# Optimization experiments

Hardware: AMD Instinct MI355X
Metric: run time of the kernel (lower is better)

## Reference

```python
import jax, jax.numpy as jnp
import numpy as np

N, FEAT, D, H, C, FF, PH, E = 50000, 64, 128, 4, 32, 512, 256, 600000
LN_EPS = 1e-5
NEG_SLOPE = 0.2


def layer_norm(x, g, b):
    m = x.mean(-1, keepdims=True)
    v = ((x - m) ** 2).mean(-1, keepdims=True)
    return (x - m) * jax.lax.rsqrt(v + LN_EPS) * g + b


def gat_conv(x, edge_index, W, a_src, a_dst, bias):
    # PyG GATConv, concat=True, add_self_loops=True, negative_slope=0.2, eval mode.
    n = x.shape[0]
    h = (x @ W).reshape(n, H, C)                       # [N,H,C]
    al_s = jnp.einsum('nhc,hc->nh', h, a_src)          # [N,H]
    al_d = jnp.einsum('nhc,hc->nh', h, a_dst)
    loops = jnp.arange(n)
    src = jnp.concatenate([edge_index[0], loops])      # [E+N]
    dst = jnp.concatenate([edge_index[1], loops])
    alpha = jax.nn.leaky_relu(al_s[src] + al_d[dst], NEG_SLOPE)  # [E+N,H]
    amax = jax.lax.stop_gradient(jax.ops.segment_max(alpha, dst, num_segments=n))
    ex = jnp.exp(alpha - amax[dst])
    denom = jax.ops.segment_sum(ex, dst, num_segments=n)
    w = ex / denom[dst]                                # segment softmax over incoming edges
    msg = h[src] * w[:, :, None]                       # [E+N,H,C]
    out = jax.ops.segment_sum(msg, dst, num_segments=n).reshape(n, H * C)
    return out + bias


def encoder_layer(x, ei, W, a_s, a_d, b, W1, b1, W2, b2, g1, bt1, g2, bt2):
    h = gat_conv(x, ei, W, a_s, a_d, b)
    x = layer_norm(x + h, g1, bt1)
    f = jax.nn.relu(x @ W1 + b1) @ W2 + b2
    return layer_norm(x + f, g2, bt2)


def setup_inputs() -> dict:
    key = jax.random.key(0)
    ks = iter(jax.random.split(key, 64))
    rn = lambda shp, s=0.08: jax.random.normal(next(ks), shp, dtype=jnp.float32) * s
    d = {}
    d['x'] = jax.random.normal(next(ks), (N, FEAT), dtype=jnp.float32)
    d['edge_index'] = jax.random.randint(next(ks), (2, E), 0, N)
    d['virtual_edge_index'] = jax.random.randint(next(ks), (2, E), 0, N)
    d['Wp'] = rn((FEAT, D)); d['bp'] = jnp.zeros((D,))
    d['lnp_g'] = jnp.ones((D,)); d['lnp_b'] = jnp.zeros((D,))
    for p in ('v', 'r'):
        d[p + 'W'] = rn((2, D, D)); d[p + '_as'] = rn((2, H, C), 0.1); d[p + '_ad'] = rn((2, H, C), 0.1)
        d[p + '_b'] = jnp.zeros((2, D))
        d[p + 'W1'] = rn((2, D, FF)); d[p + 'b1'] = jnp.zeros((2, FF))
        d[p + 'W2'] = rn((2, FF, D)); d[p + 'b2'] = jnp.zeros((2, D))
        d[p + 'ln1g'] = jnp.ones((2, D)); d[p + 'ln1b'] = jnp.zeros((2, D))
        d[p + 'ln2g'] = jnp.ones((2, D)); d[p + 'ln2b'] = jnp.zeros((2, D))
    d['We1'] = rn((2 * D, PH)); d['be1'] = jnp.zeros((PH,))
    d['We2'] = rn((PH, 1)); d['be2'] = jnp.zeros((1,))
    return d


def reference(x, edge_index, virtual_edge_index, Wp, bp, lnp_g, lnp_b,
              vW, v_as, v_ad, v_b, vW1, vb1, vW2, vb2, vln1g, vln1b, vln2g, vln2b,
              rW, r_as, r_ad, r_b, rW1, rb1, rW2, rb2, rln1g, rln1b, rln2g, rln2b,
              We1, be1, We2, be2):
    # preprocessing
    h = layer_norm(jax.nn.relu(x @ Wp + bp), lnp_g, lnp_b)
    # virtual-link encoders
    for i in range(vW.shape[0]):
        h = encoder_layer(h, virtual_edge_index, vW[i], v_as[i], v_ad[i], v_b[i],
                          vW1[i], vb1[i], vW2[i], vb2[i], vln1g[i], vln1b[i], vln2g[i], vln2b[i])
    # real-link encoders
    for i in range(rW.shape[0]):
        h = encoder_layer(h, edge_index, rW[i], r_as[i], r_ad[i], r_b[i],
                          rW1[i], rb1[i], rW2[i], rb2[i], rln1g[i], rln1b[i], rln2g[i], rln2b[i])
    # edge predictor
    ef = jnp.concatenate([h[edge_index[0]], h[edge_index[1]]], axis=-1)  # [E,2D]
    flow = (jax.nn.relu(ef @ We1 + be1) @ We2 + be2)[:, 0]
    return jax.nn.relu(flow)
```

## Files before the change

### kernel.cpp

```cpp
#include <hip/hip_runtime.h>
#include <hip/hip_bf16.h>
#include <math.h>

#define NODES 50000
#define NFEAT 64
#define DIM 128
#define HEADS 4
#define CHC 32
#define FFDIM 512
#define PHDIM 256
#define NEDGE 600000
#define LN_EPS 1e-5f
#define SLOPE 0.2f

typedef __attribute__((ext_vector_type(8))) short bf16x8;
typedef __attribute__((ext_vector_type(4))) float f32x4;
typedef __attribute__((ext_vector_type(4))) unsigned short us4;

__device__ __forceinline__ unsigned short f2bf(float f) {
    __hip_bfloat16 h = __float2bfloat16(f);
    return reinterpret_cast<unsigned short&>(h);
}
__device__ __forceinline__ float bf2f(unsigned short u) {
    return __uint_as_float(((unsigned int)u) << 16);
}

__device__ __forceinline__ void ln_stats128(float val, float* red, float& mean, float& rstd) {
    float s1 = val, s2 = val * val;
#pragma unroll
    for (int off = 32; off > 0; off >>= 1) {
        s1 += __shfl_xor(s1, off, 64);
        s2 += __shfl_xor(s2, off, 64);
    }
    int wv = threadIdx.x >> 6;
    if ((threadIdx.x & 63) == 0) { red[wv * 2] = s1; red[wv * 2 + 1] = s2; }
    __syncthreads();
    float t1 = red[0] + red[2];
    float t2 = red[1] + red[3];
    mean = t1 * (1.f / 128.f);
    float var = t2 * (1.f / 128.f) - mean * mean;
    rstd = rsqrtf(var + LN_EPS);
}

__global__ void k_count2(const int* __restrict__ dstV, const int* __restrict__ dstR,
                         int* __restrict__ cntV, int* __restrict__ cntR) {
    int e = blockIdx.x * 256 + threadIdx.x;
    if (e < NEDGE) atomicAdd(&cntV[dstV[e]], 1);
    else if (e < 2 * NEDGE) atomicAdd(&cntR[dstR[e - NEDGE]], 1);
}

__global__ void k_scan2(const int* __restrict__ degV, int* __restrict__ rpV,
                        const int* __restrict__ degR, int* __restrict__ rpR) {
    __shared__ int sh[1024];
    const int* deg = blockIdx.x ? degR : degV;
    int* rp = blockIdx.x ? rpR : rpV;
    int t = threadIdx.x;
    const int per = (NODES + 1023) / 1024;
    int beg = t * per;
    int end = beg + per; if (end > NODES) end = NODES; if (beg > NODES) beg = NODES;
    int s = 0;
    for (int i = beg; i < end; i++) s += deg[i];
    sh[t] = s;
    __syncthreads();
    for (int off = 1; off < 1024; off <<= 1) {
        int v = (t >= off) ? sh[t - off] : 0;
        __syncthreads();
        sh[t] += v;
        __syncthreads();
    }
    int run = sh[t] - s;
    for (int i = beg; i < end; i++) { rp[i] = run; run += deg[i]; }
    if (t == 1023) rp[NODES] = sh[1023];
}

__global__ void k_fill2(const int* __restrict__ eiV, const int* __restrict__ eiR,
                        const int* __restrict__ rpV, const int* __restrict__ rpR,
                        int* __restrict__ cntV, int* __restrict__ cntR,
                        int* __restrict__ ciV, int* __restrict__ ciR) {
    int e = blockIdx.x * 256 + threadIdx.x;
    if (e < NEDGE) {
        int s = eiV[e], d = eiV[NEDGE + e];
        int pos = atomicAdd(&cntV[d], 1);
        ciV[rpV[d] + pos] = s;
    } else if (e < 2 * NEDGE) {
        int e2 = e - NEDGE;
        int s = eiR[e2], d = eiR[NEDGE + e2];
        int pos = atomicAdd(&cntR[d], 1);
        ciR[rpR[d] + pos] = s;
    }
}

template <int KI, int NR>
__global__ void k_wcvt2b(const float* __restrict__ inV, const float* __restrict__ inR,
                         unsigned short* __restrict__ oh, unsigned short* __restrict__ ol,
                         size_t ostride) {
    int l = blockIdx.y;
    const float* in = (l < 2 ? inV : inR) + (size_t)(l & 1) * KI * NR;
    unsigned short* ohp = oh + (size_t)l * ostride;
    unsigned short* olp = ol + (size_t)l * ostride;
    int tid = blockIdx.x * 256 + threadIdx.x;
    int n = tid / KI, k = tid % KI;
    float w = in[k * NR + n];
    unsigned short h = f2bf(w);
    ohp[tid] = h;
    olp[tid] = f2bf(w - bf2f(h));
}

__global__ void k_wcvt_pq(const float* __restrict__ We1, unsigned short* __restrict__ oh,
                          unsigned short* __restrict__ ol) {
    int tid = blockIdx.x * 256 + threadIdx.x;
    int n = tid >> 7, k = tid & 127;
    float w = (n < PHDIM) ? We1[k * PHDIM + n] : We1[(DIM + k) * PHDIM + (n - PHDIM)];
    unsigned short h = f2bf(w);
    oh[tid] = h;
    ol[tid] = f2bf(w - bf2f(h));
}

__global__ void k_preprocess(const float* __restrict__ x0, const float* __restrict__ Wp,
                             const float* __restrict__ bp, const float* __restrict__ g,
                             const float* __restrict__ b, float* __restrict__ xout) {
    __shared__ float xr[NFEAT];
    __shared__ float red[4];
    int n = blockIdx.x;
    int j = threadIdx.x;
    if (j < NFEAT) xr[j] = x0[n * NFEAT + j];
    __syncthreads();
    float acc = bp[j];
#pragma unroll
    for (int k = 0; k < NFEAT; k++) acc += xr[k] * Wp[k * DIM + j];
    acc = fmaxf(acc, 0.f);
    float mean, rstd;
    ln_stats128(acc, red, mean, rstd);
    xout[n * DIM + j] = (acc - mean) * rstd * g[j] + b[j];
}

#define XS_STRIDE 136
#define HID_STRIDE 520
#define FB_STRIDE 132
#define MFMA_BF16 __builtin_amdgcn_mfma_f32_16x16x32_bf16

__global__ void k_xw_mfma(const float* __restrict__ x,
                          const unsigned short* __restrict__ Wh,
                          const unsigned short* __restrict__ Wl,
                          const float* __restrict__ a_s, const float* __restrict__ a_d,
                          unsigned short* __restrict__ hg, float* __restrict__ als,
                          float* __restrict__ ald) {
    __shared__ __align__(16) unsigned short xsh[32 * XS_STRIDE];
    __shared__ __align__(16) unsigned short xsl[32 * XS_STRIDE];
    int t = threadIdx.x;
    int n0 = blockIdx.x * 32;

#pragma unroll
    for (int jj = 0; jj < 4; jj++) {
        int v = t + jj * 256;
        int m = v >> 5, c4 = (v & 31) * 4;
        int node = n0 + m;
        float4 f;
        if (node < NODES) f = *(const float4*)(x + (size_t)node * DIM + c4);
        else { f.x = f.y = f.z = f.w = 0.f; }
        us4 uh = {f2bf(f.x), f2bf(f.y), f2bf(f.z), f2bf(f.w)};
        us4 ul = {f2bf(f.x - bf2f(uh.x)), f2bf(f.y - bf2f(uh.y)),
                  f2bf(f.z - bf2f(uh.z)), f2bf(f.w - bf2f(uh.w))};
        *(us4*)(xsh + m * XS_STRIDE + c4) = uh;
        *(us4*)(xsl + m * XS_STRIDE + c4) = ul;
    }
    __syncthreads();

    int wv = t >> 6, l = t & 63, lr = l & 15, lk = l >> 4;

    f32x4 acc[2][2];
#pragma unroll
    for (int mf = 0; mf < 2; mf++)
#pragma unroll
        for (int nf = 0; nf < 2; nf++) acc[mf][nf] = (f32x4){0.f, 0.f, 0.f, 0.f};
#pragma unroll
    for (int kk = 0; kk < 4; kk++) {
        int c = kk * 32 + lk * 8;
        bf16x8 a0h = *(const bf16x8*)(xsh + lr * XS_STRIDE + c);
        bf16x8 a0l = *(const bf16x8*)(xsl + lr * XS_STRIDE + c);
        bf16x8 a1h = *(const bf16x8*)(xsh + (16 + lr) * XS_STRIDE + c);
        bf16x8 a1l = *(const bf16x8*)(xsl + (16 + lr) * XS_STRIDE + c);
#pragma unroll
        for (int nf = 0; nf < 2; nf++) {
            int n = wv * 32 + nf * 16 + lr;
            bf16x8 bh = *(const bf16x8*)(Wh + (size_t)n * DIM + c);
            bf16x8 bl = *(const bf16x8*)(Wl + (size_t)n * DIM + c);
            acc[0][nf] = MFMA_BF16(a0h, bh, acc[0][nf], 0, 0, 0);
            acc[0][nf] = MFMA_BF16(a0l, bh, acc[0][nf], 0, 0, 0);
            acc[0][nf] = MFMA_BF16(a0h, bl, acc[0][nf], 0, 0, 0);
            acc[1][nf] = MFMA_BF16(a1h, bh, acc[1][nf], 0, 0, 0);
            acc[1][nf] = MFMA_BF16(a1l, bh, acc[1][nf], 0, 0, 0);
            acc[1][nf] = MFMA_BF16(a1h, bl, acc[1][nf], 0, 0, 0);
        }
    }

    float as0 = a_s[wv * 32 + lr], as1 = a_s[wv * 32 + 16 + lr];
    float ad0 = a_d[wv * 32 + lr], ad1 = a_d[wv * 32 + 16 + lr];
#pragma unroll
    for (int mf = 0; mf < 2; mf++) {
#pragma unroll
        for (int r = 0; r < 4; r++) {
            int m = mf * 16 + lk * 4 + r;
            int node = n0 + m;
            float v0 = acc[mf][0][r], v1 = acc[mf][1][r];
            if (node < NODES) {
                hg[(size_t)node * DIM + wv * 32 + lr] = f2bf(v0);
                hg[(size_t)node * DIM + wv * 32 + 16 + lr] = f2bf(v1);
            }
            float ps = v0 * as0 + v1 * as1;
            float pd = v0 * ad0 + v1 * ad1;
#pragma unroll
            for (int off = 8; off > 0; off >>= 1) {
                ps += __shfl_xor(ps, off, 64);
                pd += __shfl_xor(pd, off, 64);
            }
            if (lr == 0 && node < NODES) {
                als[node * HEADS + wv] = ps;
                ald[node * HEADS + wv] = pd;
            }
        }
    }
}

__global__ void k_agg(const float* __restrict__ x, const unsigned short* __restrict__ hg,
                      const float* __restrict__ als, const float* __restrict__ ald,
                      const int* __restrict__ rp, const int* __restrict__ ci,
                      const float* __restrict__ bias, const float* __restrict__ g,
                      const float* __restrict__ b, float* __restrict__ y) {
    __shared__ float red[4];
    int n = blockIdx.x, j = threadIdx.x, head = j >> 5;
    float aldn = ald[n * HEADS + head];
    float a0 = als[n * HEADS + head] + aldn;
    a0 = (a0 > 0.f) ? a0 : SLOPE * a0;
    float ex = __expf(a0);
    float den = ex;
    float acc = ex * bf2f(hg[(size_t)n * DIM + j]);
    int beg = rp[n], end = rp[n + 1];
    int e = beg;
    for (; e + 4 <= end; e += 4) {
        int s0 = ci[e], s1 = ci[e + 1], s2 = ci[e + 2], s3 = ci[e + 3];
        float av0 = als[s0 * HEADS + head] + aldn;
        float av1 = als[s1 * HEADS + head] + aldn;
        float av2 = als[s2 * HEADS + head] + aldn;
        float av3 = als[s3 * HEADS + head] + aldn;
        av0 = (av0 > 0.f) ? av0 : SLOPE * av0;
        av1 = (av1 > 0.f) ? av1 : SLOPE * av1;
        av2 = (av2 > 0.f) ? av2 : SLOPE * av2;
        av3 = (av3 > 0.f) ? av3 : SLOPE * av3;
        float e0 = __expf(av0), e1 = __expf(av1), e2 = __expf(av2), e3 = __expf(av3);
        float h0 = bf2f(hg[(size_t)s0 * DIM + j]);
        float h1 = bf2f(hg[(size_t)s1 * DIM + j]);
        float h2 = bf2f(hg[(size_t)s2 * DIM + j]);
        float h3 = bf2f(hg[(size_t)s3 * DIM + j]);
        den += (e0 + e1) + (e2 + e3);
        acc += e0 * h0 + e1 * h1 + e2 * h2 + e3 * h3;
    }
    for (; e < end; e++) {
        int s = ci[e];
        float av = als[s * HEADS + head] + aldn;
        av = (av > 0.f) ? av : SLOPE * av;
        float e2 = __expf(av);
        den += e2;
        acc += e2 * bf2f(hg[(size_t)s * DIM + j]);
    }
    float val = x[(size_t)n * DIM + j] + acc / den + bias[j];
    float mean, rstd;
    ln_stats128(val, red, mean, rstd);
    y[(size_t)n * DIM + j] = (val - mean) * rstd * g[j] + b[j];
}

#define TM 32

__global__ void k_ffn_mfma(
    const float* __restrict__ yin,
    const unsigned short* __restrict__ W1h, const unsigned short* __restrict__ W1l,
    const float* __restrict__ b1,
    const unsigned short* __restrict__ W2h, const unsigned short* __restrict__ W2l,
    const float* __restrict__ b2, const float* __restrict__ g,
    const float* __restrict__ b, float* __restrict__ xout) {
    __shared__ __align__(16) unsigned char smem[(2 * TM * XS_STRIDE + 2 * TM * HID_STRIDE) * 2];
    unsigned short* xsh = (unsigned short*)smem;
    unsigned short* xsl = xsh + TM * XS_STRIDE;
    unsigned short* hidh = xsl + TM * XS_STRIDE;
    unsigned short* hidl = hidh + TM * HID_STRIDE;
    float* fbuf = (float*)hidh;

    int t = threadIdx.x;
    int n0 = blockIdx.x * TM;

#pragma unroll
    for (int jj = 0; jj < 2; jj++) {
        int v = t + jj * 512;
        int m = v >> 5, c4 = (v & 31) * 4;
        int node = n0 + m;
        float4 f;
        if (node < NODES) f = *(const float4*)(yin + (size_t)node * DIM + c4);
        else { f.x = f.y = f.z = f.w = 0.f; }
        us4 uh = {f2bf(f.x), f2bf(f.y), f2bf(f.z), f2bf(f.w)};
        us4 ul = {f2bf(f.x - bf2f(uh.x)), f2bf(f.y - bf2f(uh.y)),
                  f2bf(f.z - bf2f(uh.z)), f2bf(f.w - bf2f(uh.w))};
        *(us4*)(xsh + m * XS_STRIDE + c4) = uh;
        *(us4*)(xsl + m * XS_STRIDE + c4) = ul;
    }
    __syncthreads();

    int wv = t >> 6, l = t & 63, lr = l & 15, lk = l >> 4;

    {
        f32x4 acc[2][4];
#pragma unroll
        for (int mf = 0; mf < 2; mf++)
#pragma unroll
            for (int nf = 0; nf < 4; nf++) acc[mf][nf] = (f32x4){0.f, 0.f, 0.f, 0.f};
#pragma unroll
        for (int kk = 0; kk < 4; kk++) {
            int c = kk * 32 + lk * 8;
            bf16x8 a0h = *(const bf16x8*)(xsh + lr * XS_STRIDE + c);
            bf16x8 a0l = *(const bf16x8*)(xsl + lr * XS_STRIDE + c);
            bf16x8 a1h = *(const bf16x8*)(xsh + (16 + lr) * XS_STRIDE + c);
            bf16x8 a1l = *(const bf16x8*)(xsl + (16 + lr) * XS_STRIDE + c);
#pragma unroll
            for (int nf = 0; nf < 4; nf++) {
                int n = wv * 64 + nf * 16 + lr;
                bf16x8 bh = *(const bf16x8*)(W1h + (size_t)n * DIM + c);
                bf16x8 bl = *(const bf16x8*)(W1l + (size_t)n * DIM + c);
                acc[0][nf] = MFMA_BF16(a0h, bh, acc[0][nf], 0, 0, 0);
                acc[0][nf] = MFMA_BF16(a0l, bh, acc[0][nf], 0, 0, 0);
                acc[0][nf] = MFMA_BF16(a0h, bl, acc[0][nf], 0, 0, 0);
                acc[1][nf] = MFMA_BF16(a1h, bh, acc[1][nf], 0, 0, 0);
                acc[1][nf] = MFMA_BF16(a1l, bh, acc[1][nf], 0, 0, 0);
                acc[1][nf] = MFMA_BF16(a1h, bl, acc[1][nf], 0, 0, 0);
            }
        }
#pragma unroll
        for (int nf = 0; nf < 4; nf++) {
            int n = wv * 64 + nf * 16 + lr;
            float bias = b1[n];
#pragma unroll
            for (int mf = 0; mf < 2; mf++)
#pragma unroll
                for (int r = 0; r < 4; r++) {
                    int m = mf * 16 + lk * 4 + r;
                    float val = fmaxf(acc[mf][nf][r] + bias, 0.f);
                    unsigned short h = f2bf(val);
                    hidh[m * HID_STRIDE + n] = h;
                    hidl[m * HID_STRIDE + n] = f2bf(val - bf2f(h));
                }
        }
    }
    __syncthreads();

    f32x4 acc2[2];
#pragma unroll
    for (int mf = 0; mf < 2; mf++) acc2[mf] = (f32x4){0.f, 0.f, 0.f, 0.f};
#pragma unroll
    for (int kk = 0; kk < 16; kk++) {
        int c = kk * 32 + lk * 8;
        bf16x8 a0h = *(const bf16x8*)(hidh + lr * HID_STRIDE + c);
        bf16x8 a0l = *(const bf16x8*)(hidl + lr * HID_STRIDE + c);
        bf16x8 a1h = *(const bf16x8*)(hidh + (16 + lr) * HID_STRIDE + c);
        bf16x8 a1l = *(const bf16x8*)(hidl + (16 + lr) * HID_STRIDE + c);
        int n = wv * 16 + lr;
        bf16x8 bh = *(const bf16x8*)(W2h + (size_t)n * FFDIM + c);
        bf16x8 bl = *(const bf16x8*)(W2l + (size_t)n * FFDIM + c);
        acc2[0] = MFMA_BF16(a0h, bh, acc2[0], 0, 0, 0);
        acc2[0] = MFMA_BF16(a0l, bh, acc2[0], 0, 0, 0);
        acc2[0] = MFMA_BF16(a0h, bl, acc2[0], 0, 0, 0);
        acc2[1] = MFMA_BF16(a1h, bh, acc2[1], 0, 0, 0);
        acc2[1] = MFMA_BF16(a1l, bh, acc2[1], 0, 0, 0);
        acc2[1] = MFMA_BF16(a1h, bl, acc2[1], 0, 0, 0);
    }
    __syncthreads();

    {
        int n = wv * 16 + lr;
        float bias = b2[n];
#pragma unroll
        for (int mf = 0; mf < 2; mf++)
#pragma unroll
            for (int r = 0; r < 4; r++) {
                int m = mf * 16 + lk * 4 + r;
                int node = n0 + m;
                float yv = (node < NODES) ? yin[(size_t)node * DIM + n] : 0.f;
                fbuf[m * FB_STRIDE + n] = acc2[mf][r] + bias + yv;
            }
    }
    __syncthreads();

    {
        int row = t >> 4, l16 = t & 15;
        float4 vv[2];
        float s1 = 0.f, s2 = 0.f;
#pragma unroll
        for (int q = 0; q < 2; q++) {
            vv[q] = *(float4*)(fbuf + row * FB_STRIDE + l16 * 8 + q * 4);
            s1 += vv[q].x + vv[q].y + vv[q].z + vv[q].w;
            s2 += vv[q].x * vv[q].x + vv[q].y * vv[q].y + vv[q].z * vv[q].z + vv[q].w * vv[q].w;
        }
#pragma unroll
        for (int off = 8; off > 0; off >>= 1) {
            s1 += __shfl_xor(s1, off, 64);
            s2 += __shfl_xor(s2, off, 64);
        }
        float mean = s1 * (1.f / 128.f);
        float var = s2 * (1.f / 128.f) - mean * mean;
        float rstd = rsqrtf(var + LN_EPS);
        int node = n0 + row;
        if (node < NODES) {
#pragma unroll
            for (int q = 0; q < 2; q++) {
                int c = l16 * 8 + q * 4;
                float4 gv = *(const float4*)(g + c);
                float4 bv = *(const float4*)(b + c);
                float4 o;
                o.x = (vv[q].x - mean) * rstd * gv.x + bv.x;
                o.y = (vv[q].y - mean) * rstd * gv.y + bv.y;
                o.z = (vv[q].z - mean) * rstd * gv.z + bv.z;
                o.w = (vv[q].w - mean) * rstd * gv.w + bv.w;
                *(float4*)(xout + (size_t)node * DIM + c) = o;
            }
        }
    }
}

__global__ void k_pq_mfma(const float* __restrict__ x,
                          const unsigned short* __restrict__ Wh,
                          const unsigned short* __restrict__ Wl,
                          const float* __restrict__ be1,
                          __hip_bfloat16* __restrict__ P, __hip_bfloat16* __restrict__ Q) {
    __shared__ __align__(16) unsigned short xsh[32 * XS_STRIDE];
    __shared__ __align__(16) unsigned short xsl[32 * XS_STRIDE];
    int t = threadIdx.x;
    int n0 = blockIdx.x * 32;

#pragma unroll
    for (int jj = 0; jj < 4; jj++) {
        int v = t + jj * 256;
        int m = v >> 5, c4 = (v & 31) * 4;
        int node = n0 + m;
        float4 f;
        if (node < NODES) f = *(const float4*)(x + (size_t)node * DIM + c4);
        else { f.x = f.y = f.z = f.w = 0.f; }
        us4 uh = {f2bf(f.x), f2bf(f.y), f2bf(f.z), f2bf(f.w)};
        us4 ul = {f2bf(f.x - bf2f(uh.x)), f2bf(f.y - bf2f(uh.y)),
                  f2bf(f.z - bf2f(uh.z)), f2bf(f.w - bf2f(uh.w))};
        *(us4*)(xsh + m * XS_STRIDE + c4) = uh;
        *(us4*)(xsl + m * XS_STRIDE + c4) = ul;
    }
    __syncthreads();

    int wv = t >> 6, l = t & 63, lr = l & 15, lk = l >> 4;

    f32x4 acc[2][8];
#pragma unroll
    for (int mf = 0; mf < 2; mf++)
#pragma unroll
        for (int nf = 0; nf < 8; nf++) acc[mf][nf] = (f32x4){0.f, 0.f, 0.f, 0.f};
#pragma unroll
    for (int kk = 0; kk < 4; kk++) {
        int c = kk * 32 + lk * 8;
        bf16x8 a0h = *(const bf16x8*)(xsh + lr * XS_STRIDE + c);
        bf16x8 a0l = *(const bf16x8*)(xsl + lr * XS_STRIDE + c);
        bf16x8 a1h = *(const bf16x8*)(xsh + (16 + lr) * XS_STRIDE + c);
        bf16x8 a1l = *(const bf16x8*)(xsl + (16 + lr) * XS_STRIDE + c);
#pragma unroll
        for (int nf = 0; nf < 8; nf++) {
            int n = wv * 128 + nf * 16 + lr;
            bf16x8 bh = *(const bf16x8*)(Wh + (size_t)n * DIM + c);
            bf16x8 bl = *(const bf16x8*)(Wl + (size_t)n * DIM + c);
            acc[0][nf] = MFMA_BF16(a0h, bh, acc[0][nf], 0, 0, 0);
            acc[0][nf] = MFMA_BF16(a0l, bh, acc[0][nf], 0, 0, 0);
            acc[0][nf] = MFMA_BF16(a0h, bl, acc[0][nf], 0, 0, 0);
            acc[1][nf] = MFMA_BF16(a1h, bh, acc[1][nf], 0, 0, 0);
            acc[1][nf] = MFMA_BF16(a1l, bh, acc[1][nf], 0, 0, 0);
            acc[1][nf] = MFMA_BF16(a1h, bl, acc[1][nf], 0, 0, 0);
        }
    }

#pragma unroll
    for (int nf = 0; nf < 8; nf++) {
        int n = wv * 128 + nf * 16 + lr;
        float bias = (n < PHDIM) ? be1[n] : 0.f;
        __hip_bfloat16* dst = (n < PHDIM) ? P : Q;
        int col = n & (PHDIM - 1);
#pragma unroll
        for (int mf = 0; mf < 2; mf++)
#pragma unroll
            for (int r = 0; r < 4; r++) {
                int m = mf * 16 + lk * 4 + r;
                int node = n0 + m;
                if (node < NODES)
                    dst[(size_t)node * PHDIM + col] = __float2bfloat16(acc[mf][nf][r] + bias);
            }
    }
}

__global__ void k_edge(const int* __restrict__ ei, const __hip_bfloat16* __restrict__ P,
                       const __hip_bfloat16* __restrict__ Q, const float* __restrict__ We2,
                       const float* __restrict__ be2, float* __restrict__ out) {
    int lane = threadIdx.x & 63;
    int wv = threadIdx.x >> 6;
    int e = blockIdx.x * 8 + wv;
    if (e >= NEDGE) return;
    float4 w2 = ((const float4*)We2)[lane];
    int s = ei[e], d = ei[NEDGE + e];
    uint2 pu = ((const uint2*)P)[(size_t)s * 64 + lane];
    uint2 qu = ((const uint2*)Q)[(size_t)d * 64 + lane];
    float p0 = __uint_as_float(pu.x << 16);
    float p1 = __uint_as_float(pu.x & 0xffff0000u);
    float p2 = __uint_as_float(pu.y << 16);
    float p3 = __uint_as_float(pu.y & 0xffff0000u);
    float q0 = __uint_as_float(qu.x << 16);
    float q1 = __uint_as_float(qu.x & 0xffff0000u);
    float q2 = __uint_as_float(qu.y << 16);
    float q3 = __uint_as_float(qu.y & 0xffff0000u);
    float acc = fmaxf(p0 + q0, 0.f) * w2.x + fmaxf(p1 + q1, 0.f) * w2.y +
                fmaxf(p2 + q2, 0.f) * w2.z + fmaxf(p3 + q3, 0.f) * w2.w;
#pragma unroll
    for (int off = 32; off > 0; off >>= 1) acc += __shfl_xor(acc, off, 64);
    if (lane == 0) out[e] = fmaxf(acc + be2[0], 0.f);
}

extern "C" void kernel_launch(void* const* d_in, const int* in_sizes, int n_in,
                              void* d_out, int out_size, void* d_ws, size_t ws_size,
                              hipStream_t stream) {
    const float* x0   = (const float*)d_in[0];
    const int*   eiR  = (const int*)d_in[1];
    const int*   eiV  = (const int*)d_in[2];
    const float* Wp   = (const float*)d_in[3];
    const float* bp   = (const float*)d_in[4];
    const float* lnpg = (const float*)d_in[5];
    const float* lnpb = (const float*)d_in[6];
    const float* vW   = (const float*)d_in[7];
    const float* v_as = (const float*)d_in[8];
    const float* v_ad = (const float*)d_in[9];
    const float* v_b  = (const float*)d_in[10];
    const float* vW1  = (const float*)d_in[11];
    const float* vb1  = (const float*)d_in[12];
    const float* vW2  = (const float*)d_in[13];
    const float* vb2  = (const float*)d_in[14];
    const float* vln1g = (const float*)d_in[15];
    const float* vln1b = (const float*)d_in[16];
    const float* vln2g = (const float*)d_in[17];
    const float* vln2b = (const float*)d_in[18];
    const float* rW   = (const float*)d_in[19];
    const float* r_as = (const float*)d_in[20];
    const float* r_ad = (const float*)d_in[21];
    const float* r_b  = (const float*)d_in[22];
    const float* rW1  = (const float*)d_in[23];
    const float* rb1  = (const float*)d_in[24];
    const float* rW2  = (const float*)d_in[25];
    const float* rb2  = (const float*)d_in[26];
    const float* rln1g = (const float*)d_in[27];
    const float* rln1b = (const float*)d_in[28];
    const float* rln2g = (const float*)d_in[29];
    const float* rln2b = (const float*)d_in[30];
    const float* We1  = (const float*)d_in[31];
    const float* be1  = (const float*)d_in[32];
    const float* We2  = (const float*)d_in[33];
    const float* be2  = (const float*)d_in[34];
    float* out = (float*)d_out;

    float* X   = (float*)d_ws;
    float* Y   = X + (size_t)NODES * DIM;
    unsigned short* HG = (unsigned short*)(Y + (size_t)NODES * DIM);
    float* ALS = (float*)(HG + (size_t)NODES * DIM);
    float* ALD = ALS + (size_t)NODES * HEADS;
    __hip_bfloat16* Pb = (__hip_bfloat16*)(ALD + (size_t)NODES * HEADS);
    __hip_bfloat16* Qb = Pb + (size_t)NODES * PHDIM;
    unsigned short* WT = (unsigned short*)(Qb + (size_t)NODES * PHDIM);
    unsigned short* WXT = WT + (size_t)4 * 4 * 65536;
    unsigned short* WPQ = WXT + (size_t)4 * 2 * 16384;
    int* rpV = (int*)(WPQ + (size_t)2 * 65536);
    int* ciV = rpV + (NODES + 1);
    int* rpR = ciV + NEDGE;
    int* ciR = rpR + (NODES + 1);
    int* cntV = ciR + NEDGE;
    int* cntR = cntV + NODES;

    const int EB2 = (2 * NEDGE + 255) / 256;

    hipMemsetAsync(cntV, 0, sizeof(int) * 2 * NODES, stream);
    k_count2<<<EB2, 256, 0, stream>>>(eiV + NEDGE, eiR + NEDGE, cntV, cntR);
    k_scan2<<<2, 1024, 0, stream>>>(cntV, rpV, cntR, rpR);
    hipMemsetAsync(cntV, 0, sizeof(int) * 2 * NODES, stream);
    k_fill2<<<EB2, 256, 0, stream>>>(eiV, eiR, rpV, rpR, cntV, cntR, ciV, ciR);

    {
        dim3 g1(256, 4);
        k_wcvt2b<DIM, FFDIM><<<g1, 256, 0, stream>>>(vW1, rW1, WT, WT + 65536, 262144);
        dim3 g2(256, 4);
        k_wcvt2b<FFDIM, DIM><<<g2, 256, 0, stream>>>(vW2, rW2, WT + 131072, WT + 196608, 262144);
        dim3 g3(64, 4);
        k_wcvt2b<DIM, DIM><<<g3, 256, 0, stream>>>(vW, rW, WXT, WXT + 16384, 32768);
        k_wcvt_pq<<<256, 256, 0, stream>>>(We1, WPQ, WPQ + 65536);
    }

    k_preprocess<<<NODES, 128, 0, stream>>>(x0, Wp, bp, lnpg, lnpb, X);

    for (int l = 0; l < 4; l++) {
        bool virt = (l < 2);
        int i = virt ? l : (l - 2);
        const float* As = (virt ? v_as : r_as) + (size_t)i * HEADS * CHC;
        const float* Ad = (virt ? v_ad : r_ad) + (size_t)i * HEADS * CHC;
        const float* Bb = (virt ? v_b : r_b) + (size_t)i * DIM;
        const float* B1 = (virt ? vb1 : rb1) + (size_t)i * FFDIM;
        const float* B2 = (virt ? vb2 : rb2) + (size_t)i * DIM;
        const float* G1 = (virt ? vln1g : rln1g) + (size_t)i * DIM;
        const float* B1n = (virt ? vln1b : rln1b) + (size_t)i * DIM;
        const float* G2 = (virt ? vln2g : rln2g) + (size_t)i * DIM;
        const float* B2n = (virt ? vln2b : rln2b) + (size_t)i * DIM;
        const int* rp = virt ? rpV : rpR;
        const int* ci = virt ? ciV : ciR;

        unsigned short* bx = WXT + (size_t)l * 32768;
        k_xw_mfma<<<(NODES + 31) / 32, 256, 0, stream>>>(X, bx, bx + 16384, As, Ad, HG, ALS, ALD);
        k_agg<<<NODES, 128, 0, stream>>>(X, HG, ALS, ALD, rp, ci, Bb, G1, B1n, Y);
        unsigned short* base = WT + (size_t)l * 262144;
        k_ffn_mfma<<<(NODES + TM - 1) / TM, 512, 0, stream>>>(
            Y, base, base + 65536, B1, base + 131072, base + 196608, B2, G2, B2n, X);
    }

    k_pq_mfma<<<(NODES + 31) / 32, 256, 0, stream>>>(X, WPQ, WPQ + 65536, be1, Pb, Qb);
    k_edge<<<(NEDGE + 7) / 8, 512, 0, stream>>>(eiR, Pb, Qb, We2, be2, out);
}
```

Baseline: 1.265 ms.

## Split fused FFN into hidden-write and second-GEMM kernels with fp16 hidden

Replaces the single fused FFN kernel, which kept a 32x512 hidden tile in LDS as bf16 hi/lo pairs, with two kernels. The first computes relu(yW1+b1) and writes the hidden activations to global memory as fp16. The second streams that hidden tensor in 128-wide chunks and does the W2 GEMM with fp16 MFMA, splitting only the weights into hi/lo, so it needs 2 MFMAs per step instead of 3. This cuts the large LDS footprint and the MFMA count to raise occupancy, but adds a global round trip of N x 512 fp16 per layer and an fp16 precision risk on the hidden values.

```diff
diff --git a/kernel.cpp b/kernel.cpp
--- a/kernel.cpp
+++ b/kernel.cpp
@@ -14,6 +14,7 @@
 #define SLOPE 0.2f
 
 typedef __attribute__((ext_vector_type(8))) short bf16x8;
+typedef __attribute__((ext_vector_type(8))) _Float16 f16x8;
 typedef __attribute__((ext_vector_type(4))) float f32x4;
 typedef __attribute__((ext_vector_type(4))) unsigned short us4;
 
@@ -23,6 +24,14 @@
 }
 __device__ __forceinline__ float bf2f(unsigned short u) {
     return __uint_as_float(((unsigned int)u) << 16);
+}
+__device__ __forceinline__ unsigned short f2h(float f) {
+    _Float16 h = (_Float16)f;
+    return reinterpret_cast<unsigned short&>(h);
+}
+__device__ __forceinline__ float h2f(unsigned short u) {
+    _Float16 h = reinterpret_cast<_Float16&>(u);
+    return (float)h;
 }
 
 __device__ __forceinline__ void ln_stats128(float val, float* red, float& mean, float& rstd) {
@@ -106,6 +115,22 @@
     olp[tid] = f2bf(w - bf2f(h));
 }
 
+template <int KI, int NR>
+__global__ void k_wcvt2h(const float* __restrict__ inV, const float* __restrict__ inR,
+                         unsigned short* __restrict__ oh, unsigned short* __restrict__ ol,
+                         size_t ostride) {
+    int l = blockIdx.y;
+    const float* in = (l < 2 ? inV : inR) + (size_t)(l & 1) * KI * NR;
+    unsigned short* ohp = oh + (size_t)l * ostride;
+    unsigned short* olp = ol + (size_t)l * ostride;
+    int tid = blockIdx.x * 256 + threadIdx.x;
+    int n = tid / KI, k = tid % KI;
+    float w = in[k * NR + n];
+    unsigned short h = f2h(w);
+    ohp[tid] = h;
+    olp[tid] = f2h(w - h2f(h));
+}
+
 __global__ void k_wcvt_pq(const float* __restrict__ We1, unsigned short* __restrict__ oh,
                           unsigned short* __restrict__ ol) {
     int tid = blockIdx.x * 256 + threadIdx.x;
@@ -135,9 +160,9 @@
 }
 
 #define XS_STRIDE 136
-#define HID_STRIDE 520
 #define FB_STRIDE 132
 #define MFMA_BF16 __builtin_amdgcn_mfma_f32_16x16x32_bf16
+#define MFMA_F16  __builtin_amdgcn_mfma_f32_16x16x32_f16
 
 __global__ void k_xw_mfma(const float* __restrict__ x,
                           const unsigned short* __restrict__ Wh,
@@ -269,32 +294,23 @@
     y[(size_t)n * DIM + j] = (val - mean) * rstd * g[j] + b[j];
 }
 
-#define TM 32
-
-__global__ void k_ffn_mfma(
-    const float* __restrict__ yin,
-    const unsigned short* __restrict__ W1h, const unsigned short* __restrict__ W1l,
-    const float* __restrict__ b1,
-    const unsigned short* __restrict__ W2h, const unsigned short* __restrict__ W2l,
-    const float* __restrict__ b2, const float* __restrict__ g,
-    const float* __restrict__ b, float* __restrict__ xout) {
-    __shared__ __align__(16) unsigned char smem[(2 * TM * XS_STRIDE + 2 * TM * HID_STRIDE) * 2];
-    unsigned short* xsh = (unsigned short*)smem;
-    unsigned short* xsl = xsh + TM * XS_STRIDE;
-    unsigned short* hidh = xsl + TM * XS_STRIDE;
-    unsigned short* hidl = hidh + TM * HID_STRIDE;
-    float* fbuf = (float*)hidh;
-
+__global__ void k_hid(const float* __restrict__ y,
+                      const unsigned short* __restrict__ W1h,
+                      const unsigned short* __restrict__ W1l,
+                      const float* __restrict__ b1,
+                      unsigned short* __restrict__ hid) {
+    __shared__ __align__(16) unsigned short xsh[32 * XS_STRIDE];
+    __shared__ __align__(16) unsigned short xsl[32 * XS_STRIDE];
     int t = threadIdx.x;
-    int n0 = blockIdx.x * TM;
-
-#pragma unroll
-    for (int jj = 0; jj < 2; jj++) {
-        int v = t + jj * 512;
+    int n0 = blockIdx.x * 32;
+
+#pragma unroll
+    for (int jj = 0; jj < 4; jj++) {
+        int v = t + jj * 256;
         int m = v >> 5, c4 = (v & 31) * 4;
         int node = n0 + m;
         float4 f;
-        if (node < NODES) f = *(const float4*)(yin + (size_t)node * DIM + c4);
+        if (node < NODES) f = *(const float4*)(y + (size_t)node * DIM + c4);
         else { f.x = f.y = f.z = f.w = 0.f; }
         us4 uh = {f2bf(f.x), f2bf(f.y), f2bf(f.z), f2bf(f.w)};
         us4 ul = {f2bf(f.x - bf2f(uh.x)), f2bf(f.y - bf2f(uh.y)),
@@ -306,74 +322,101 @@
 
     int wv = t >> 6, l = t & 63, lr = l & 15, lk = l >> 4;
 
-    {
-        f32x4 acc[2][4];
+    f32x4 acc[2][8];
+#pragma unroll
+    for (int mf = 0; mf < 2; mf++)
+#pragma unroll
+        for (int nf = 0; nf < 8; nf++) acc[mf][nf] = (f32x4){0.f, 0.f, 0.f, 0.f};
+#pragma unroll
+    for (int kk = 0; kk < 4; kk++) {
+        int c = kk * 32 + lk * 8;
+        bf16x8 a0h = *(const bf16x8*)(xsh + lr * XS_STRIDE + c);
+        bf16x8 a0l = *(const bf16x8*)(xsl + lr * XS_STRIDE + c);
+        bf16x8 a1h = *(const bf16x8*)(xsh + (16 + lr) * XS_STRIDE + c);
+        bf16x8 a1l = *(const bf16x8*)(xsl + (16 + lr) * XS_STRIDE + c);
+#pragma unroll
+        for (int nf = 0; nf < 8; nf++) {
+            int n = wv * 128 + nf * 16 + lr;
+            bf16x8 bh = *(const bf16x8*)(W1h + (size_t)n * DIM + c);
+            bf16x8 bl = *(const bf16x8*)(W1l + (size_t)n * DIM + c);
+            acc[0][nf] = MFMA_BF16(a0h, bh, acc[0][nf], 0, 0, 0);
+            acc[0][nf] = MFMA_BF16(a0l, bh, acc[0][nf], 0, 0, 0);
+            acc[0][nf] = MFMA_BF16(a0h, bl, acc[0][nf], 0, 0, 0);
+            acc[1][nf] = MFMA_BF16(a1h, bh, acc[1][nf], 0, 0, 0);
+            acc[1][nf] = MFMA_BF16(a1l, bh, acc[1][nf], 0, 0, 0);
+            acc[1][nf] = MFMA_BF16(a1h, bl, acc[1][nf], 0, 0, 0);
+        }
+    }
+
+#pragma unroll
+    for (int nf = 0; nf < 8; nf++) {
+        int n = wv * 128 + nf * 16 + lr;
+        float bias = b1[n];
 #pragma unroll
         for (int mf = 0; mf < 2; mf++)
 #pragma unroll
-            for (int nf = 0; nf < 4; nf++) acc[mf][nf] = (f32x4){0.f, 0.f, 0.f, 0.f};
+            for (int r = 0; r < 4; r++) {
+                int m = mf * 16 + lk * 4 + r;
+                int node = n0 + m;
+                if (node < NODES)
+                    hid[(size_t)node * FFDIM + n] = f2h(fmaxf(acc[mf][nf][r] + bias, 0.f));
+            }
+    }
+}
+
+__global__ void k_ffn2(const float* __restrict__ yin,
+                       const unsigned short* __restrict__ hid,
+                       const unsigned short* __restrict__ W2h,
+                       const unsigned short* __restrict__ W2l,
+                       const float* __restrict__ b2, const float* __restrict__ g,
+                       const float* __restrict__ b, float* __restrict__ xout) {
+    __shared__ __align__(16) unsigned short hs[32 * XS_STRIDE];
+    __shared__ float fbuf[32 * FB_STRIDE];
+    int t = threadIdx.x;
+    int n0 = blockIdx.x * 32;
+    int wv = t >> 6, l = t & 63, lr = l & 15, lk = l >> 4;
+
+    f32x4 acc[2][2];
+#pragma unroll
+    for (int mf = 0; mf < 2; mf++)
+#pragma unroll
+        for (int nf = 0; nf < 2; nf++) acc[mf][nf] = (f32x4){0.f, 0.f, 0.f, 0.f};
+
+    for (int ck = 0; ck < 4; ck++) {
+#pragma unroll
+        for (int jj = 0; jj < 2; jj++) {
+            int v = t + jj * 256;
+            int m = v >> 4, c8 = (v & 15) * 8;
+            int node = n0 + m;
+            f16x8 hv = {0, 0, 0, 0, 0, 0, 0, 0};
+            if (node < NODES)
+                hv = *(const f16x8*)(hid + (size_t)node * FFDIM + ck * 128 + c8);
+            *(f16x8*)(hs + m * XS_STRIDE + c8) = hv;
+        }
+        __syncthreads();
 #pragma unroll
         for (int kk = 0; kk < 4; kk++) {
             int c = kk * 32 + lk * 8;
-            bf16x8 a0h = *(const bf16x8*)(xsh + lr * XS_STRIDE + c);
-            bf16x8 a0l = *(const bf16x8*)(xsl + lr * XS_STRIDE + c);
-            bf16x8 a1h = *(const bf16x8*)(xsh + (16 + lr) * XS_STRIDE + c);
-            bf16x8 a1l = *(const bf16x8*)(xsl + (16 + lr) * XS_STRIDE + c);
-#pragma unroll
-            for (int nf = 0; nf < 4; nf++) {
-                int n = wv * 64 + nf * 16 + lr;
-                bf16x8 bh = *(const bf16x8*)(W1h + (size_t)n * DIM + c);
-                bf16x8 bl = *(const bf16x8*)(W1l + (size_t)n * DIM + c);
-                acc[0][nf] = MFMA_BF16(a0h, bh, acc[0][nf], 0, 0, 0);
-                acc[0][nf] = MFMA_BF16(a0l, bh, acc[0][nf], 0, 0, 0);
-                acc[0][nf] = MFMA_BF16(a0h, bl, acc[0][nf], 0, 0, 0);
-                acc[1][nf] = MFMA_BF16(a1h, bh, acc[1][nf], 0, 0, 0);
-                acc[1][nf] = MFMA_BF16(a1l, bh, acc[1][nf], 0, 0, 0);
-                acc[1][nf] = MFMA_BF16(a1h, bl, acc[1][nf], 0, 0, 0);
-            }
-        }
-#pragma unroll
-        for (int nf = 0; nf < 4; nf++) {
-            int n = wv * 64 + nf * 16 + lr;
-            float bias = b1[n];
-#pragma unroll
-            for (int mf = 0; mf < 2; mf++)
-#pragma unroll
-                for (int r = 0; r < 4; r++) {
-                    int m = mf * 16 + lk * 4 + r;
-                    float val = fmaxf(acc[mf][nf][r] + bias, 0.f);
-                    unsigned short h = f2bf(val);
-                    hidh[m * HID_STRIDE + n] = h;
-                    hidl[m * HID_STRIDE + n] = f2bf(val - bf2f(h));
-                }
-        }
-    }
-    __syncthreads();
-
-    f32x4 acc2[2];
-#pragma unroll
-    for (int mf = 0; mf < 2; mf++) acc2[mf] = (f32x4){0.f, 0.f, 0.f, 0.f};
-#pragma unroll
-    for (int kk = 0; kk < 16; kk++) {
-        int c = kk * 32 + lk * 8;
-        bf16x8 a0h = *(const bf16x8*)(hidh + lr * HID_STRIDE + c);
-        bf16x8 a0l = *(const bf16x8*)(hidl + lr * HID_STRIDE + c);
-        bf16x8 a1h = *(const bf16x8*)(hidh + (16 + lr) * HID_STRIDE + c);
-        bf16x8 a1l = *(const bf16x8*)(hidl + (16 + lr) * HID_STRIDE + c);
-        int n = wv * 16 + lr;
-        bf16x8 bh = *(const bf16x8*)(W2h + (size_t)n * FFDIM + c);
-        bf16x8 bl = *(const bf16x8*)(W2l + (size_t)n * FFDIM + c);
-        acc2[0] = MFMA_BF16(a0h, bh, acc2[0], 0, 0, 0);
-        acc2[0] = MFMA_BF16(a0l, bh, acc2[0], 0, 0, 0);
-        acc2[0] = MFMA_BF16(a0h, bl, acc2[0], 0, 0, 0);
-        acc2[1] = MFMA_BF16(a1h, bh, acc2[1], 0, 0, 0);
-        acc2[1] = MFMA_BF16(a1l, bh, acc2[1], 0, 0, 0);
-        acc2[1] = MFMA_BF16(a1h, bl, acc2[1], 0, 0, 0);
-    }
-    __syncthreads();
-
-    {
-        int n = wv * 16 + lr;
+            f16x8 a0 = *(const f16x8*)(hs + lr * XS_STRIDE + c);
+            f16x8 a1 = *(const f16x8*)(hs + (16 + lr) * XS_STRIDE + c);
+#pragma unroll
+            for (int nf = 0; nf < 2; nf++) {
+                int n = wv * 32 + nf * 16 + lr;
+                int kb = ck * 128 + c;
+                f16x8 bh = *(const f16x8*)(W2h + (size_t)n * FFDIM + kb);
+                f16x8 bl = *(const f16x8*)(W2l + (size_t)n * FFDIM + kb);
+                acc[0][nf] = MFMA_F16(a0, bh, acc[0][nf], 0, 0, 0);
+                acc[0][nf] = MFMA_F16(a0, bl, acc[0][nf], 0, 0, 0);
+                acc[1][nf] = MFMA_F16(a1, bh, acc[1][nf], 0, 0, 0);
+                acc[1][nf] = MFMA_F16(a1, bl, acc[1][nf], 0, 0, 0);
+            }
+        }
+        __syncthreads();
+    }
+
+#pragma unroll
+    for (int nf = 0; nf < 2; nf++) {
+        int n = wv * 32 + nf * 16 + lr;
         float bias = b2[n];
 #pragma unroll
         for (int mf = 0; mf < 2; mf++)
@@ -382,23 +425,23 @@
                 int m = mf * 16 + lk * 4 + r;
                 int node = n0 + m;
                 float yv = (node < NODES) ? yin[(size_t)node * DIM + n] : 0.f;
-                fbuf[m * FB_STRIDE + n] = acc2[mf][r] + bias + yv;
+                fbuf[m * FB_STRIDE + n] = acc[mf][nf][r] + bias + yv;
             }
     }
     __syncthreads();
 
     {
-        int row = t >> 4, l16 = t & 15;
-        float4 vv[2];
+        int row = t >> 3, l8 = t & 7;
+        float4 vv[4];
         float s1 = 0.f, s2 = 0.f;
 #pragma unroll
-        for (int q = 0; q < 2; q++) {
-            vv[q] = *(float4*)(fbuf + row * FB_STRIDE + l16 * 8 + q * 4);
+        for (int q = 0; q < 4; q++) {
+            vv[q] = *(float4*)(fbuf + row * FB_STRIDE + l8 * 16 + q * 4);
             s1 += vv[q].x + vv[q].y + vv[q].z + vv[q].w;
             s2 += vv[q].x * vv[q].x + vv[q].y * vv[q].y + vv[q].z * vv[q].z + vv[q].w * vv[q].w;
         }
 #pragma unroll
-        for (int off = 8; off > 0; off >>= 1) {
+        for (int off = 4; off > 0; off >>= 1) {
             s1 += __shfl_xor(s1, off, 64);
             s2 += __shfl_xor(s2, off, 64);
         }
@@ -408,8 +451,8 @@
         int node = n0 + row;
         if (node < NODES) {
 #pragma unroll
-            for (int q = 0; q < 2; q++) {
-                int c = l16 * 8 + q * 4;
+            for (int q = 0; q < 4; q++) {
+                int c = l8 * 16 + q * 4;
                 float4 gv = *(const float4*)(g + c);
                 float4 bv = *(const float4*)(b + c);
                 float4 o;
@@ -568,6 +611,7 @@
     float* ALD = ALS + (size_t)NODES * HEADS;
     __hip_bfloat16* Pb = (__hip_bfloat16*)(ALD + (size_t)NODES * HEADS);
     __hip_bfloat16* Qb = Pb + (size_t)NODES * PHDIM;
+    unsigned short* HID = (unsigned short*)Pb;
     unsigned short* WT = (unsigned short*)(Qb + (size_t)NODES * PHDIM);
     unsigned short* WXT = WT + (size_t)4 * 4 * 65536;
     unsigned short* WPQ = WXT + (size_t)4 * 2 * 16384;
@@ -590,13 +634,15 @@
         dim3 g1(256, 4);
         k_wcvt2b<DIM, FFDIM><<<g1, 256, 0, stream>>>(vW1, rW1, WT, WT + 65536, 262144);
         dim3 g2(256, 4);
-        k_wcvt2b<FFDIM, DIM><<<g2, 256, 0, stream>>>(vW2, rW2, WT + 131072, WT + 196608, 262144);
+        k_wcvt2h<FFDIM, DIM><<<g2, 256, 0, stream>>>(vW2, rW2, WT + 131072, WT + 196608, 262144);
         dim3 g3(64, 4);
         k_wcvt2b<DIM, DIM><<<g3, 256, 0, stream>>>(vW, rW, WXT, WXT + 16384, 32768);
         k_wcvt_pq<<<256, 256, 0, stream>>>(We1, WPQ, WPQ + 65536);
     }
 
     k_preprocess<<<NODES, 128, 0, stream>>>(x0, Wp, bp, lnpg, lnpb, X);
+
+    const int NB32 = (NODES + 31) / 32;
 
     for (int l = 0; l < 4; l++) {
         bool virt = (l < 2);
@@ -614,13 +660,13 @@
         const int* ci = virt ? ciV : ciR;
 
         unsigned short* bx = WXT + (size_t)l * 32768;
-        k_xw_mfma<<<(NODES + 31) / 32, 256, 0, stream>>>(X, bx, bx + 16384, As, Ad, HG, ALS, ALD);
+        k_xw_mfma<<<NB32, 256, 0, stream>>>(X, bx, bx + 16384, As, Ad, HG, ALS, ALD);
         k_agg<<<NODES, 128, 0, stream>>>(X, HG, ALS, ALD, rp, ci, Bb, G1, B1n, Y);
         unsigned short* base = WT + (size_t)l * 262144;
-        k_ffn_mfma<<<(NODES + TM - 1) / TM, 512, 0, stream>>>(
-            Y, base, base + 65536, B1, base + 131072, base + 196608, B2, G2, B2n, X);
-    }
-
-    k_pq_mfma<<<(NODES + 31) / 32, 256, 0, stream>>>(X, WPQ, WPQ + 65536, be1, Pb, Qb);
+        k_hid<<<NB32, 256, 0, stream>>>(Y, base, base + 65536, B1, HID);
+        k_ffn2<<<NB32, 256, 0, stream>>>(Y, HID, base + 131072, base + 196608, B2, G2, B2n, X);
+    }
+
+    k_pq_mfma<<<NB32, 256, 0, stream>>>(X, WPQ, WPQ + 65536, be1, Pb, Qb);
     k_edge<<<(NEDGE + 7) / 8, 512, 0, stream>>>(eiR, Pb, Qb, We2, be2, out);
 }
```

Measured after the change: 1.332 ms. 1.05x slower.
